# Kernel tuning notes

Hardware: AMD Instinct MI355X
Metric: run time of the kernel (lower is better)

## Reference

```python
import jax, jax.numpy as jnp
import numpy as np

M, K, N = 131072, 512, 512


def setup_inputs() -> dict:
    key = jax.random.key(0)
    k1, k2, k3, k4 = jax.random.split(key, 4)
    # Simulated int8 quantized values held in float32 (real kernel uses int8)
    x = jnp.round(jax.random.normal(k1, (M, K), dtype=jnp.float32) * 30.0)
    weight = jnp.round(jax.random.normal(k2, (N, K), dtype=jnp.float32) * 30.0)
    # per-token activation scale [M,1], per-output-channel weight scale [N]
    x_scale = jax.random.uniform(k3, (M, 1), dtype=jnp.float32, minval=1e-3, maxval=2e-2)
    weight_scale = jax.random.uniform(k4, (N,), dtype=jnp.float32, minval=1e-3, maxval=2e-2)
    return {"x": x, "x_scale": x_scale, "weight": weight, "weight_scale": weight_scale}


def reference(x, x_scale, weight, weight_scale):
    # gemm_a8w8(per_Token): out[m,n] = (sum_k x[m,k]*W[n,k]) * x_scale[m] * w_scale[n]
    acc = jnp.einsum('mk,nk->mn', x, weight)          # [M, N] int32-equivalent accum
    out = acc * x_scale * weight_scale[None, :]       # fused dequant scaling
    return out  # otype would be bf16 in the original; kept fp32 as reference baseline
```

## Files before the change

### kernel.cpp

```cpp
#include <hip/hip_runtime.h>
#include <hip/hip_bf16.h>
#include <stdint.h>

#define K_DIM 512
#define N_DIM 512
#define BM 64

typedef __bf16 bf16x8 __attribute__((ext_vector_type(8)));
typedef float floatx4 __attribute__((ext_vector_type(4)));

__device__ __forceinline__ bf16x8 cvt8(float4 a, float4 b) {
    bf16x8 r;
    r[0] = (__bf16)a.x; r[1] = (__bf16)a.y; r[2] = (__bf16)a.z; r[3] = (__bf16)a.w;
    r[4] = (__bf16)b.x; r[5] = (__bf16)b.y; r[6] = (__bf16)b.z; r[7] = (__bf16)b.w;
    return r;
}

__global__ __launch_bounds__(512) void wconv_kernel(const float* __restrict__ w,
                                                    __bf16* __restrict__ wf) {
    int t = blockIdx.x * 512 + threadIdx.x;
    int lane = t & 63, slot = t >> 6;
    int n = ((slot >> 4) << 4) + (lane & 15);
    int k = ((slot & 15) << 5) + ((lane >> 4) << 3);
    const float* src = w + (size_t)n * K_DIM + k;
    float4 f0 = *(const float4*)src;
    float4 f1 = *(const float4*)(src + 4);
    *(bf16x8*)(wf + (size_t)t * 8) = cvt8(f0, f1);
}

template <bool USE_WF>
__global__ __launch_bounds__(512, 4) void gemm_kernel(
    const float* __restrict__ x, const float* __restrict__ xscale,
    const __bf16* __restrict__ wf, const float* __restrict__ w,
    const float* __restrict__ wscale, float* __restrict__ out)
{
    __shared__ __bf16 lds[BM * K_DIM];
    const int t = threadIdx.x;
    const int lane = t & 63;
    const int wid = t >> 6;
    const int rowb = blockIdx.x * BM;

    #pragma unroll
    for (int p = 0; p < 8; ++p) {
        int idx = p * 8 + wid;
        int rt = idx >> 4, kc = idx & 15;
        int row = (rt << 4) + (lane & 15);
        int k = (kc << 5) + ((lane >> 4) << 3);
        const float* src = x + (size_t)(rowb + row) * K_DIM + k;
        float4 f0 = *(const float4*)src;
        float4 f1 = *(const float4*)(src + 4);
        *(bf16x8*)&lds[idx * 512 + lane * 8] = cvt8(f0, f1);
    }
    __syncthreads();

    const int colb = wid * 64;
    floatx4 acc[4][4];
    #pragma unroll
    for (int i = 0; i < 4; ++i)
        #pragma unroll
        for (int j = 0; j < 4; ++j) acc[i][j] = (floatx4)0.f;

    for (int kc = 0; kc < 16; ++kc) {
        bf16x8 ax[4];
        #pragma unroll
        for (int rt = 0; rt < 4; ++rt)
            ax[rt] = *(const bf16x8*)&lds[((rt << 4) + kc) * 512 + lane * 8];
        #pragma unroll
        for (int nt = 0; nt < 4; ++nt) {
            bf16x8 bw;
            if (USE_WF) {
                int ntg = (wid << 2) + nt;
                bw = *(const bf16x8*)(wf + (size_t)(((ntg << 4) + kc) * 64 + lane) * 8);
            } else {
                int n = colb + (nt << 4) + (lane & 15);
                int k = (kc << 5) + ((lane >> 4) << 3);
                const float* src = w + (size_t)n * K_DIM + k;
                float4 f0 = *(const float4*)src;
                float4 f1 = *(const float4*)(src + 4);
                bw = cvt8(f0, f1);
            }
            #pragma unroll
            for (int rt = 0; rt < 4; ++rt)
                acc[rt][nt] = __builtin_amdgcn_mfma_f32_16x16x32_bf16(bw, ax[rt], acc[rt][nt], 0, 0, 0);
        }
    }

    #pragma unroll
    for (int rt = 0; rt < 4; ++rt) {
        int m = rowb + (rt << 4) + (lane & 15);
        float xs = xscale[m];
        #pragma unroll
        for (int nt = 0; nt < 4; ++nt) {
            int nb = colb + (nt << 4) + ((lane >> 4) << 2);
            float4 wsc = *(const float4*)(wscale + nb);
            floatx4 a = acc[rt][nt];
            float4 o;
            o.x = a[0] * xs * wsc.x;
            o.y = a[1] * xs * wsc.y;
            o.z = a[2] * xs * wsc.z;
            o.w = a[3] * xs * wsc.w;
            *(float4*)(out + (size_t)m * N_DIM + nb) = o;
        }
    }
}

extern "C" void kernel_launch(void* const* d_in, const int* in_sizes, int n_in,
                              void* d_out, int out_size, void* d_ws, size_t ws_size,
                              hipStream_t stream) {
    const float* x      = (const float*)d_in[0];
    const float* xscale = (const float*)d_in[1];
    const float* w      = (const float*)d_in[2];
    const float* wscale = (const float*)d_in[3];
    float* out          = (float*)d_out;

    const int M = in_sizes[0] / K_DIM;
    const int grid = M / BM;

    if (ws_size >= (size_t)(N_DIM * K_DIM * sizeof(unsigned short))) {
        __bf16* wf = (__bf16*)d_ws;
        wconv_kernel<<<dim3(64), dim3(512), 0, stream>>>(w, wf);
        gemm_kernel<true><<<dim3(grid), dim3(512), 0, stream>>>(x, xscale, wf, w, wscale, out);
    } else {
        gemm_kernel<false><<<dim3(grid), dim3(512), 0, stream>>>(x, xscale, nullptr, w, wscale, out);
    }
}
```

Before: 187.0 us.

## Persistent 1024-thread blocks with register-prefetched next tile into LDS halves

Replaces the one-tile-per-block grid with 256 persistent blocks of 1024 threads, each looping over consecutive 64-row tiles. Each wave now covers 32 output columns instead of 64. While the current tile is computed, the next tile's x data is prefetched into registers and written into whichever LDS half has already been consumed. The goal is to hide global load latency and launch overhead behind the MFMA work. The cost is extra barriers per tile, more register pressure, and roughly one block per CU, which lowers the number of waves available to hide latency.

After: 407.5 us. 2.18x slower.

```diff
diff --git a/kernel.cpp b/kernel.cpp
--- a/kernel.cpp
+++ b/kernel.cpp
@@ -29,77 +29,155 @@
 }
 
 template <bool USE_WF>
-__global__ __launch_bounds__(512, 4) void gemm_kernel(
+__global__ __launch_bounds__(1024, 4) void gemm_kernel(
     const float* __restrict__ x, const float* __restrict__ xscale,
     const __bf16* __restrict__ wf, const float* __restrict__ w,
-    const float* __restrict__ wscale, float* __restrict__ out)
+    const float* __restrict__ wscale, float* __restrict__ out,
+    int ntiles, int tilesPerBlock)
 {
     __shared__ __bf16 lds[BM * K_DIM];
     const int t = threadIdx.x;
     const int lane = t & 63;
     const int wid = t >> 6;
-    const int rowb = blockIdx.x * BM;
-
-    #pragma unroll
-    for (int p = 0; p < 8; ++p) {
-        int idx = p * 8 + wid;
-        int rt = idx >> 4, kc = idx & 15;
-        int row = (rt << 4) + (lane & 15);
-        int k = (kc << 5) + ((lane >> 4) << 3);
-        const float* src = x + (size_t)(rowb + row) * K_DIM + k;
-        float4 f0 = *(const float4*)src;
-        float4 f1 = *(const float4*)(src + 4);
-        *(bf16x8*)&lds[idx * 512 + lane * 8] = cvt8(f0, f1);
+    const int laneR = lane & 15;
+    const int laneK = (lane >> 4) << 3;
+    const int colb = wid * 32;
+
+    const int tile0 = blockIdx.x * tilesPerBlock;
+    if (tile0 >= ntiles) return;
+    const int tileEnd = (tile0 + tilesPerBlock < ntiles) ? (tile0 + tilesPerBlock) : ntiles;
+
+    {
+        float4 f[8];
+        #pragma unroll
+        for (int p = 0; p < 4; ++p) {
+            int slot = wid * 4 + p;
+            int rt = slot >> 4, kc = slot & 15;
+            const float* src = x + (size_t)(tile0 * BM + rt * 16 + laneR) * K_DIM + kc * 32 + laneK;
+            f[2 * p]     = *(const float4*)src;
+            f[2 * p + 1] = *(const float4*)(src + 4);
+        }
+        #pragma unroll
+        for (int p = 0; p < 4; ++p) {
+            int slot = wid * 4 + p;
+            *(bf16x8*)&lds[slot * 512 + lane * 8] = cvt8(f[2 * p], f[2 * p + 1]);
+        }
     }
     __syncthreads();
 
-    const int colb = wid * 64;
-    floatx4 acc[4][4];
-    #pragma unroll
-    for (int i = 0; i < 4; ++i)
-        #pragma unroll
-        for (int j = 0; j < 4; ++j) acc[i][j] = (floatx4)0.f;
-
-    for (int kc = 0; kc < 16; ++kc) {
-        bf16x8 ax[4];
-        #pragma unroll
-        for (int rt = 0; rt < 4; ++rt)
-            ax[rt] = *(const bf16x8*)&lds[((rt << 4) + kc) * 512 + lane * 8];
-        #pragma unroll
-        for (int nt = 0; nt < 4; ++nt) {
-            bf16x8 bw;
-            if (USE_WF) {
-                int ntg = (wid << 2) + nt;
-                bw = *(const bf16x8*)(wf + (size_t)(((ntg << 4) + kc) * 64 + lane) * 8);
-            } else {
-                int n = colb + (nt << 4) + (lane & 15);
-                int k = (kc << 5) + ((lane >> 4) << 3);
-                const float* src = w + (size_t)n * K_DIM + k;
-                float4 f0 = *(const float4*)src;
-                float4 f1 = *(const float4*)(src + 4);
-                bw = cvt8(f0, f1);
-            }
+    floatx4 acc[4][2];
+
+    for (int tile = tile0; tile < tileEnd; ++tile) {
+        const int rowb = tile * BM;
+        const bool pf = (tile + 1 < tileEnd);
+        float4 r0[4], r1[4];
+
+        if (pf) {
+            #pragma unroll
+            for (int p = 0; p < 2; ++p) {
+                int s2 = wid * 2 + p;
+                int rt = s2 >> 3, kc = s2 & 7;
+                const float* src = x + (size_t)((tile + 1) * BM + rt * 16 + laneR) * K_DIM + kc * 32 + laneK;
+                r0[2 * p]     = *(const float4*)src;
+                r0[2 * p + 1] = *(const float4*)(src + 4);
+            }
+        }
+
+        #pragma unroll
+        for (int i = 0; i < 4; ++i) { acc[i][0] = (floatx4)0.f; acc[i][1] = (floatx4)0.f; }
+
+        #pragma unroll
+        for (int kc = 0; kc < 8; ++kc) {
+            bf16x8 ax[4];
             #pragma unroll
             for (int rt = 0; rt < 4; ++rt)
-                acc[rt][nt] = __builtin_amdgcn_mfma_f32_16x16x32_bf16(bw, ax[rt], acc[rt][nt], 0, 0, 0);
-        }
-    }
-
-    #pragma unroll
-    for (int rt = 0; rt < 4; ++rt) {
-        int m = rowb + (rt << 4) + (lane & 15);
-        float xs = xscale[m];
-        #pragma unroll
-        for (int nt = 0; nt < 4; ++nt) {
-            int nb = colb + (nt << 4) + ((lane >> 4) << 2);
-            float4 wsc = *(const float4*)(wscale + nb);
-            floatx4 a = acc[rt][nt];
-            float4 o;
-            o.x = a[0] * xs * wsc.x;
-            o.y = a[1] * xs * wsc.y;
-            o.z = a[2] * xs * wsc.z;
-            o.w = a[3] * xs * wsc.w;
-            *(float4*)(out + (size_t)m * N_DIM + nb) = o;
+                ax[rt] = *(const bf16x8*)&lds[(rt * 16 + kc) * 512 + lane * 8];
+            #pragma unroll
+            for (int nt = 0; nt < 2; ++nt) {
+                bf16x8 bw;
+                if (USE_WF) {
+                    int ntg = (wid << 1) + nt;
+                    bw = *(const bf16x8*)(wf + (size_t)(((ntg << 4) + kc) * 64 + lane) * 8);
+                } else {
+                    int n = colb + (nt << 4) + laneR;
+                    const float* src = w + (size_t)n * K_DIM + (kc << 5) + laneK;
+                    bw = cvt8(*(const float4*)src, *(const float4*)(src + 4));
+                }
+                #pragma unroll
+                for (int rt = 0; rt < 4; ++rt)
+                    acc[rt][nt] = __builtin_amdgcn_mfma_f32_16x16x32_bf16(bw, ax[rt], acc[rt][nt], 0, 0, 0);
+            }
+        }
+
+        __syncthreads();
+
+        if (pf) {
+            #pragma unroll
+            for (int p = 0; p < 2; ++p) {
+                int s2 = wid * 2 + p;
+                int rt = s2 >> 3, kc = s2 & 7;
+                *(bf16x8*)&lds[(rt * 16 + kc) * 512 + lane * 8] = cvt8(r0[2 * p], r0[2 * p + 1]);
+            }
+            #pragma unroll
+            for (int p = 0; p < 2; ++p) {
+                int s2 = wid * 2 + p;
+                int rt = s2 >> 3, kc = 8 + (s2 & 7);
+                const float* src = x + (size_t)((tile + 1) * BM + rt * 16 + laneR) * K_DIM + kc * 32 + laneK;
+                r1[2 * p]     = *(const float4*)src;
+                r1[2 * p + 1] = *(const float4*)(src + 4);
+            }
+        }
+
+        #pragma unroll
+        for (int kc = 8; kc < 16; ++kc) {
+            bf16x8 ax[4];
+            #pragma unroll
+            for (int rt = 0; rt < 4; ++rt)
+                ax[rt] = *(const bf16x8*)&lds[(rt * 16 + kc) * 512 + lane * 8];
+            #pragma unroll
+            for (int nt = 0; nt < 2; ++nt) {
+                bf16x8 bw;
+                if (USE_WF) {
+                    int ntg = (wid << 1) + nt;
+                    bw = *(const bf16x8*)(wf + (size_t)(((ntg << 4) + kc) * 64 + lane) * 8);
+                } else {
+                    int n = colb + (nt << 4) + laneR;
+                    const float* src = w + (size_t)n * K_DIM + (kc << 5) + laneK;
+                    bw = cvt8(*(const float4*)src, *(const float4*)(src + 4));
+                }
+                #pragma unroll
+                for (int rt = 0; rt < 4; ++rt)
+                    acc[rt][nt] = __builtin_amdgcn_mfma_f32_16x16x32_bf16(bw, ax[rt], acc[rt][nt], 0, 0, 0);
+            }
+        }
+
+        #pragma unroll
+        for (int rt = 0; rt < 4; ++rt) {
+            int m = rowb + rt * 16 + laneR;
+            float xs = xscale[m];
+            #pragma unroll
+            for (int nt = 0; nt < 2; ++nt) {
+                int nb = colb + (nt << 4) + ((lane >> 4) << 2);
+                float4 wsc = *(const float4*)(wscale + nb);
+                floatx4 a = acc[rt][nt];
+                float4 o;
+                o.x = a[0] * xs * wsc.x;
+                o.y = a[1] * xs * wsc.y;
+                o.z = a[2] * xs * wsc.z;
+                o.w = a[3] * xs * wsc.w;
+                *(float4*)(out + (size_t)m * N_DIM + nb) = o;
+            }
+        }
+
+        __syncthreads();
+
+        if (pf) {
+            #pragma unroll
+            for (int p = 0; p < 2; ++p) {
+                int s2 = wid * 2 + p;
+                int rt = s2 >> 3, kc = 8 + (s2 & 7);
+                *(bf16x8*)&lds[(rt * 16 + kc) * 512 + lane * 8] = cvt8(r1[2 * p], r1[2 * p + 1]);
+            }
         }
     }
 }
@@ -114,13 +192,17 @@
     float* out          = (float*)d_out;
 
     const int M = in_sizes[0] / K_DIM;
-    const int grid = M / BM;
+    const int ntiles = M / BM;
+    const int nblocks = (ntiles < 256) ? ntiles : 256;
+    const int tpb = (ntiles + nblocks - 1) / nblocks;
 
     if (ws_size >= (size_t)(N_DIM * K_DIM * sizeof(unsigned short))) {
-        __bf16* wf = (__bf16*)d_ws;
-        wconv_kernel<<<dim3(64), dim3(512), 0, stream>>>(w, wf);
-        gemm_kernel<true><<<dim3(grid), dim3(512), 0, stream>>>(x, xscale, wf, w, wscale, out);
+        __bf16* wfp = (__bf16*)d_ws;
+        wconv_kernel<<<dim3(64), dim3(512), 0, stream>>>(w, wfp);
+        gemm_kernel<true><<<dim3(nblocks), dim3(1024), 0, stream>>>(
+            x, xscale, wfp, w, wscale, out, ntiles, tpb);
     } else {
-        gemm_kernel<false><<<dim3(grid), dim3(512), 0, stream>>>(x, xscale, nullptr, w, wscale, out);
+        gemm_kernel<false><<<dim3(nblocks), dim3(1024), 0, stream>>>(
+            x, xscale, nullptr, w, wscale, out, ntiles, tpb);
     }
 }
```

## Persistent blocks with double-buffered async global-to-LDS staging of activations

Applied to the files above, without the earlier changes.

Replaces the one-tile-per-block launch with a persistent grid of up to 512 blocks, each looping over several 64-row tiles. Activations are streamed as fp32 in 128-wide K chunks straight into LDS via global_load_lds, with double buffering and an XOR swizzle, and are converted to bf16 at fragment-read time. The aim is to overlap the x loads with MFMA work and cut LDS footprint. The cost is doing the fp32-to-bf16 conversion in the inner loop and adding hand-written waitcnt/barrier synchronisation, which could be fragile.

New measurement: 297.3 us. 58.9% more time.

```diff
diff --git a/kernel.cpp b/kernel.cpp
--- a/kernel.cpp
+++ b/kernel.cpp
@@ -5,6 +5,8 @@
 #define K_DIM 512
 #define N_DIM 512
 #define BM 64
+#define CHUNK_K 128
+#define CHUNK_FLOATS (BM * CHUNK_K)
 
 typedef __bf16 bf16x8 __attribute__((ext_vector_type(8)));
 typedef float floatx4 __attribute__((ext_vector_type(4)));
@@ -28,78 +30,121 @@
     *(bf16x8*)(wf + (size_t)t * 8) = cvt8(f0, f1);
 }
 
+__device__ __forceinline__ void stage_chunk(const float* __restrict__ x,
+                                            int rowBase, int kBase,
+                                            float* ldsBuf, int wid, int lane) {
+    #pragma unroll
+    for (int i = 0; i < 4; ++i) {
+        int sl = i * 8 + wid;
+        int row = sl * 2 + (lane >> 5);
+        int srcByte = ((lane & 31) * 16) ^ ((row & 7) << 4);
+        const float* g = x + (size_t)(rowBase + row) * K_DIM + kBase + (srcByte >> 2);
+        float* l = ldsBuf + sl * 256;
+        __builtin_amdgcn_global_load_lds(
+            (const __attribute__((address_space(1))) void*)g,
+            (__attribute__((address_space(3))) void*)l, 16, 0, 0);
+    }
+}
+
+__device__ __forceinline__ bf16x8 read_afrag(const float* ldsBuf, int rt, int kcl, int lane) {
+    int row = rt * 16 + (lane & 15);
+    int sw = (row & 7) << 4;
+    int b0 = kcl * 128 + ((lane >> 4) << 5);
+    const char* rb = (const char*)(ldsBuf + row * CHUNK_K);
+    float4 fa = *(const float4*)(rb + (b0 ^ sw));
+    float4 fb = *(const float4*)(rb + ((b0 + 16) ^ sw));
+    return cvt8(fa, fb);
+}
+
 template <bool USE_WF>
 __global__ __launch_bounds__(512, 4) void gemm_kernel(
     const float* __restrict__ x, const float* __restrict__ xscale,
     const __bf16* __restrict__ wf, const float* __restrict__ w,
-    const float* __restrict__ wscale, float* __restrict__ out)
+    const float* __restrict__ wscale, float* __restrict__ out,
+    int ntiles, int tilesPerBlock)
 {
-    __shared__ __bf16 lds[BM * K_DIM];
+    __shared__ float lds[2 * CHUNK_FLOATS];
     const int t = threadIdx.x;
     const int lane = t & 63;
     const int wid = t >> 6;
-    const int rowb = blockIdx.x * BM;
+    const int laneR = lane & 15;
+    const int colb = wid * 64;
 
-    #pragma unroll
-    for (int p = 0; p < 8; ++p) {
-        int idx = p * 8 + wid;
-        int rt = idx >> 4, kc = idx & 15;
-        int row = (rt << 4) + (lane & 15);
-        int k = (kc << 5) + ((lane >> 4) << 3);
-        const float* src = x + (size_t)(rowb + row) * K_DIM + k;
-        float4 f0 = *(const float4*)src;
-        float4 f1 = *(const float4*)(src + 4);
-        *(bf16x8*)&lds[idx * 512 + lane * 8] = cvt8(f0, f1);
-    }
-    __syncthreads();
+    const int tile0 = blockIdx.x * tilesPerBlock;
+    if (tile0 >= ntiles) return;
+    const int tileEnd = (tile0 + tilesPerBlock < ntiles) ? (tile0 + tilesPerBlock) : ntiles;
+    const int nChunks = (tileEnd - tile0) * 4;
 
-    const int colb = wid * 64;
     floatx4 acc[4][4];
-    #pragma unroll
-    for (int i = 0; i < 4; ++i)
+
+    stage_chunk(x, tile0 * BM, 0, &lds[0], wid, lane);
+
+    for (int c = 0; c < nChunks; ++c) {
+        const int tile = tile0 + (c >> 2);
+
+        if (c > 0)
+            asm volatile("s_waitcnt lgkmcnt(0)\n\ts_barrier" ::: "memory");
+
+        if (c + 1 < nChunks) {
+            int cn = c + 1;
+            stage_chunk(x, (tile0 + (cn >> 2)) * BM, (cn & 3) * CHUNK_K,
+                        &lds[(cn & 1) * CHUNK_FLOATS], wid, lane);
+            asm volatile("s_waitcnt vmcnt(4)\n\ts_barrier" ::: "memory");
+        } else {
+            asm volatile("s_waitcnt vmcnt(0)\n\ts_barrier" ::: "memory");
+        }
+
+        if ((c & 3) == 0) {
+            #pragma unroll
+            for (int i = 0; i < 4; ++i)
+                #pragma unroll
+                for (int j = 0; j < 4; ++j) acc[i][j] = (floatx4)0.f;
+        }
+
+        const float* cb = &lds[(c & 1) * CHUNK_FLOATS];
         #pragma unroll
-        for (int j = 0; j < 4; ++j) acc[i][j] = (floatx4)0.f;
-
-    for (int kc = 0; kc < 16; ++kc) {
-        bf16x8 ax[4];
-        #pragma unroll
-        for (int rt = 0; rt < 4; ++rt)
-            ax[rt] = *(const bf16x8*)&lds[((rt << 4) + kc) * 512 + lane * 8];
-        #pragma unroll
-        for (int nt = 0; nt < 4; ++nt) {
-            bf16x8 bw;
-            if (USE_WF) {
-                int ntg = (wid << 2) + nt;
-                bw = *(const bf16x8*)(wf + (size_t)(((ntg << 4) + kc) * 64 + lane) * 8);
-            } else {
-                int n = colb + (nt << 4) + (lane & 15);
-                int k = (kc << 5) + ((lane >> 4) << 3);
-                const float* src = w + (size_t)n * K_DIM + k;
-                float4 f0 = *(const float4*)src;
-                float4 f1 = *(const float4*)(src + 4);
-                bw = cvt8(f0, f1);
-            }
+        for (int kcl = 0; kcl < 4; ++kcl) {
+            const int kcg = (c & 3) * 4 + kcl;
+            bf16x8 ax[4];
             #pragma unroll
             for (int rt = 0; rt < 4; ++rt)
-                acc[rt][nt] = __builtin_amdgcn_mfma_f32_16x16x32_bf16(bw, ax[rt], acc[rt][nt], 0, 0, 0);
+                ax[rt] = read_afrag(cb, rt, kcl, lane);
+            #pragma unroll
+            for (int nt = 0; nt < 4; ++nt) {
+                bf16x8 bw;
+                if (USE_WF) {
+                    int ntg = (wid << 2) + nt;
+                    bw = *(const bf16x8*)(wf + (size_t)(((ntg << 4) + kcg) * 64 + lane) * 8);
+                } else {
+                    int n = colb + (nt << 4) + laneR;
+                    const float* src = w + (size_t)n * K_DIM + (kcg << 5) + ((lane >> 4) << 3);
+                    bw = cvt8(*(const float4*)src, *(const float4*)(src + 4));
+                }
+                #pragma unroll
+                for (int rt = 0; rt < 4; ++rt)
+                    acc[rt][nt] = __builtin_amdgcn_mfma_f32_16x16x32_bf16(bw, ax[rt], acc[rt][nt], 0, 0, 0);
+            }
         }
-    }
 
-    #pragma unroll
-    for (int rt = 0; rt < 4; ++rt) {
-        int m = rowb + (rt << 4) + (lane & 15);
-        float xs = xscale[m];
-        #pragma unroll
-        for (int nt = 0; nt < 4; ++nt) {
-            int nb = colb + (nt << 4) + ((lane >> 4) << 2);
-            float4 wsc = *(const float4*)(wscale + nb);
-            floatx4 a = acc[rt][nt];
-            float4 o;
-            o.x = a[0] * xs * wsc.x;
-            o.y = a[1] * xs * wsc.y;
-            o.z = a[2] * xs * wsc.z;
-            o.w = a[3] * xs * wsc.w;
-            *(float4*)(out + (size_t)m * N_DIM + nb) = o;
+        if ((c & 3) == 3) {
+            const int rowb = tile * BM;
+            #pragma unroll
+            for (int rt = 0; rt < 4; ++rt) {
+                int m = rowb + rt * 16 + laneR;
+                float xs = xscale[m];
+                #pragma unroll
+                for (int nt = 0; nt < 4; ++nt) {
+                    int nb = colb + (nt << 4) + ((lane >> 4) << 2);
+                    float4 wsc = *(const float4*)(wscale + nb);
+                    floatx4 a = acc[rt][nt];
+                    float4 o;
+                    o.x = a[0] * xs * wsc.x;
+                    o.y = a[1] * xs * wsc.y;
+                    o.z = a[2] * xs * wsc.z;
+                    o.w = a[3] * xs * wsc.w;
+                    *(float4*)(out + (size_t)m * N_DIM + nb) = o;
+                }
+            }
         }
     }
 }
@@ -114,13 +159,17 @@
     float* out          = (float*)d_out;
 
     const int M = in_sizes[0] / K_DIM;
-    const int grid = M / BM;
+    const int ntiles = M / BM;
+    const int nblocks = (ntiles < 512) ? ntiles : 512;
+    const int tpb = (ntiles + nblocks - 1) / nblocks;
 
     if (ws_size >= (size_t)(N_DIM * K_DIM * sizeof(unsigned short))) {
-        __bf16* wf = (__bf16*)d_ws;
-        wconv_kernel<<<dim3(64), dim3(512), 0, stream>>>(w, wf);
-        gemm_kernel<true><<<dim3(grid), dim3(512), 0, stream>>>(x, xscale, wf, w, wscale, out);
+        __bf16* wfp = (__bf16*)d_ws;
+        wconv_kernel<<<dim3(64), dim3(512), 0, stream>>>(w, wfp);
+        gemm_kernel<true><<<dim3(nblocks), dim3(512), 0, stream>>>(
+            x, xscale, wfp, w, wscale, out, ntiles, tpb);
     } else {
-        gemm_kernel<false><<<dim3(grid), dim3(512), 0, stream>>>(x, xscale, nullptr, w, wscale, out);
+        gemm_kernel<false><<<dim3(nblocks), dim3(512), 0, stream>>>(
+            x, xscale, nullptr, w, wscale, out, ntiles, tpb);
     }
 }
```
